# Performance work log

Measured on AMD Instinct MI355X. Metric: run time of the kernel, lower is better.

Reference implementation:

```python
import jax, jax.numpy as jnp
import numpy as np

EPS = 1e-7  # keras.backend.epsilon()


def setup_inputs() -> dict:
    key = jax.random.key(0)
    k1, k2, k3 = jax.random.split(key, 3)
    B, N, D_in, C, D_out = 32, 2048, 8, 32, 16
    x = jax.random.normal(k1, (B, N, D_in), dtype=jnp.float32)
    W = jax.random.normal(k2, (1, N, C, D_out, D_in), dtype=jnp.float32) * 0.05
    R = jax.random.normal(k3, (1, N, C), dtype=jnp.float32)
    return {"x": x, "W": W, "R": R}


def reference(x, W, R):
    # x: [B, N, D_in]; W: [1, N, C, D_out, D_in]; R: [1, N, C]
    R_nor = jax.nn.softmax(R[0], axis=0)          # softmax over N (axis=1 of [1,N,C])
    # per-capsule transform: u[b,n,c,j] = sum_k W[n,c,j,k] * x[b,n,k]
    u = jnp.einsum('ncjk,bnk->bncj', W[0], x)
    # routing-weighted aggregation over input capsules n
    s = jnp.einsum('bncj,nc->bcj', u, R_nor)      # [B, C, D_out]
    # squash along capsule dim (original axis=-2 before squeeze == D_out)
    ss = jnp.sum(jnp.square(s), axis=-1, keepdims=True) + EPS
    scale = jnp.sqrt(ss) / (1.0 + ss)
    return scale * s                               # [B, C, D_out]
```

## Files before the change

kernel.cpp:

```cpp
#include <hip/hip_runtime.h>
#include <math.h>


#define NN 2048
#define CC 32

__device__ __forceinline__ void g2l16(const float* g, float* l) {
  __builtin_amdgcn_global_load_lds((const __attribute__((address_space(1))) void*)g,
                                   (__attribute__((address_space(3))) void*)l, 16, 0, 0);
}

__global__ __launch_bounds__(512) __attribute__((amdgpu_waves_per_eu(4, 4)))
void caps_main(const float* __restrict__ x, const float* __restrict__ W,
               const float* __restrict__ R, float* __restrict__ P) {
  const int bid = blockIdx.x;
  const int cq = bid & 7;
  const int chunk = bid >> 3;
  const int n0 = chunk * 32;
  const int tid = threadIdx.x;
  const int ws = tid >> 6;
  const int lane = tid & 63;
  const int j = lane & 15;
  const int bo = lane >> 4;

  extern __shared__ float smem[];
  float* ldsW = smem;
  float* ldsX = smem + 8192;
  float* red8 = smem + 4096;

#pragma unroll
  for (int it = 0; it < 2; ++it) {
    int idx = it * 512 + tid;
    int nl = idx >> 7, S = idx & 127;
    int g = S ^ (((S >> 2) ^ (S >> 4)) & 1) ^ (((S >> 3) & 1) << 1) ^ (((S >> 4) & 1) << 2);
    g2l16(W + (size_t)(n0 + nl) * 4096 + cq * 512 + g * 4,
          ldsW + (size_t)(it * 512 + ws * 64) * 4);
  }

  float4 xg[4];
  int xoff[4];
#pragma unroll
  for (int it = 0; it < 4; ++it) {
    int idx = it * 512 + tid;
    int nl = idx >> 6, r = idx & 63;
    int b = r & 31, kq = r >> 5;
    xg[it] = *(const float4*)(x + (size_t)b * (NN * 8) + (size_t)(n0 + nl) * 8 + kq * 4);
    xoff[it] = nl * 256 + kq * 128 + b;
  }
#pragma unroll
  for (int it = 0; it < 4; ++it) {
    float* d = ldsX + xoff[it];
    d[0] = xg[it].x; d[32] = xg[it].y; d[64] = xg[it].z; d[96] = xg[it].w;
  }

  float se[4] = {0.f, 0.f, 0.f, 0.f};
#pragma unroll
  for (int i = 0; i < 4; ++i) {
    int n = i * 512 + tid;
    float4 a = *(const float4*)(R + (size_t)n * CC + cq * 4);
    se[0] += expf(a.x); se[1] += expf(a.y); se[2] += expf(a.z); se[3] += expf(a.w);
  }
#pragma unroll
  for (int ci = 0; ci < 4; ++ci) {
    float v = se[ci];
#pragma unroll
    for (int d = 32; d >= 1; d >>= 1) v += __shfl_xor(v, d, 64);
    se[ci] = v;
  }
  if (lane == 0) {
#pragma unroll
    for (int ci = 0; ci < 4; ++ci) red8[ws * 4 + ci] = se[ci];
  }
  __syncthreads();

  float inv4[4];
  {
    float t[4] = {0.f, 0.f, 0.f, 0.f};
#pragma unroll
    for (int w = 0; w < 8; ++w)
#pragma unroll
      for (int ci = 0; ci < 4; ++ci) t[ci] += red8[w * 4 + ci];
#pragma unroll
    for (int ci = 0; ci < 4; ++ci) inv4[ci] = 1.0f / t[ci];
  }
  __syncthreads();

  float acc[4][8];
#pragma unroll
  for (int a = 0; a < 4; ++a)
#pragma unroll
    for (int b = 0; b < 8; ++b) acc[a][b] = 0.f;

  const int jsw = j >> 1;

#pragma unroll 1
  for (int s = 0; s < 4; ++s) {
    if (s < 3) {
      const int sb = n0 + (s + 1) * 8;
      float* wdst = ldsW + (size_t)((s + 1) & 1) * 4096;
#pragma unroll
      for (int it = 0; it < 2; ++it) {
        int idx = it * 512 + tid;
        int nl = idx >> 7, S = idx & 127;
        int g = S ^ (((S >> 2) ^ (S >> 4)) & 1) ^ (((S >> 3) & 1) << 1) ^ (((S >> 4) & 1) << 2);
        g2l16(W + (size_t)(sb + nl) * 4096 + cq * 512 + g * 4,
              wdst + (size_t)(it * 512 + ws * 64) * 4);
      }
    }
    const int n = n0 + s * 8 + ws;
    const float* Xn = ldsX + (size_t)(s * 8 + ws) * 256;
    const float* Wn = ldsW + (size_t)(s & 1) * 4096 + (size_t)ws * 512;

    const float* rr = R + (size_t)n * CC + cq * 4;
    float rv[4];
#pragma unroll
    for (int ci = 0; ci < 4; ++ci) rv[ci] = expf(rr[ci]) * inv4[ci];

#pragma unroll
    for (int kh = 0; kh < 2; ++kh) {
      float4 xlo[4], xhi[4];
#pragma unroll
      for (int kk = 0; kk < 4; ++kk) {
        const float* xp = Xn + (kh * 4 + kk) * 32 + bo * 8;
        xlo[kk] = *(const float4*)xp;
        xhi[kk] = *(const float4*)(xp + 4);
      }
#pragma unroll
      for (int ci = 0; ci < 4; ++ci) {
        int slot = (ci * 32 + j * 2 + kh) ^ jsw;
        float4 wf = *(const float4*)(Wn + slot * 4);
        float rvv = rv[ci];
        float w0 = wf.x * rvv, w1 = wf.y * rvv, w2 = wf.z * rvv, w3 = wf.w * rvv;
        float a0, a1;
#pragma unroll
        for (int bi = 0; bi < 4; ++bi) {
          a0 = acc[ci][bi];
          a0 = fmaf(w0, (&xlo[0].x)[bi], a0);
          a0 = fmaf(w1, (&xlo[1].x)[bi], a0);
          a0 = fmaf(w2, (&xlo[2].x)[bi], a0);
          a0 = fmaf(w3, (&xlo[3].x)[bi], a0);
          acc[ci][bi] = a0;
          a1 = acc[ci][bi + 4];
          a1 = fmaf(w0, (&xhi[0].x)[bi], a1);
          a1 = fmaf(w1, (&xhi[1].x)[bi], a1);
          a1 = fmaf(w2, (&xhi[2].x)[bi], a1);
          a1 = fmaf(w3, (&xhi[3].x)[bi], a1);
          acc[ci][bi + 4] = a1;
        }
      }
    }
    __syncthreads();
  }

  float* red = smem;
#pragma unroll
  for (int half = 4; half >= 1; half >>= 1) {
    if (ws >= half && ws < 2 * half) {
      float* dst = red + (size_t)(ws - half) * 2048;
#pragma unroll
      for (int ci = 0; ci < 4; ++ci)
#pragma unroll
        for (int bi = 0; bi < 8; ++bi)
          dst[(ci * 8 + bi) * 64 + lane] = acc[ci][bi];
    }
    __syncthreads();
    if (ws < half) {
      const float* srcp = red + (size_t)ws * 2048;
#pragma unroll
      for (int ci = 0; ci < 4; ++ci)
#pragma unroll
        for (int bi = 0; bi < 8; ++bi)
          acc[ci][bi] += srcp[(ci * 8 + bi) * 64 + lane];
    }
    __syncthreads();
  }

  if (ws == 0) {
    float* dst = P + (size_t)bid * 2048;
#pragma unroll
    for (int ci = 0; ci < 4; ++ci)
#pragma unroll
      for (int bi = 0; bi < 8; ++bi)
        dst[(ci * 8 + bi) * 64 + lane] = acc[ci][bi];
  }
}

__global__ void caps_reduce(const float* __restrict__ P, float* __restrict__ out) {
  const int g = blockIdx.x * 256 + threadIdx.x;
  const int j = g & 15;
  const int c = (g >> 4) & 31;
  const int b = g >> 9;
  const int bo = b >> 3, bi = b & 7;
  const int cgi = c >> 2, ci = c & 3;
  const int idx = (ci * 8 + bi) * 64 + (bo * 16 + j);

  float s = 0.f;
#pragma unroll 16
  for (int ch = 0; ch < 64; ++ch) {
    s += P[(size_t)(ch * 8 + cgi) * 2048 + idx];
  }
  float sq = s * s;
  sq += __shfl_xor(sq, 8, 16);
  sq += __shfl_xor(sq, 4, 16);
  sq += __shfl_xor(sq, 2, 16);
  sq += __shfl_xor(sq, 1, 16);
  float ss = sq + 1e-7f;
  float scale = sqrtf(ss) / (1.0f + ss);
  out[g] = scale * s;
}

extern "C" void kernel_launch(void* const* d_in, const int* in_sizes, int n_in,
                              void* d_out, int out_size, void* d_ws, size_t ws_size,
                              hipStream_t stream) {
  const float* x = (const float*)d_in[0];
  const float* W = (const float*)d_in[1];
  const float* R = (const float*)d_in[2];
  float* out = (float*)d_out;
  float* P = (float*)d_ws;

  hipFuncSetAttribute((const void*)caps_main,
                      hipFuncAttributeMaxDynamicSharedMemorySize, 65536);

  caps_main<<<512, 512, 65536, stream>>>(x, W, R, P);
  caps_reduce<<<64, 256, 0, stream>>>(P, out);
}
```

Baseline: 28.42 us.

## Replace tree LDS reduction with single-pass float4 reduction and remap block indexing

The end-of-kernel cross-wave reduction used to be a three-level tree with six barriers. It becomes a single pass: all eight waves write their partials to LDS, then every thread sums eight float4 values and writes them to the workspace cooperatively. This cuts barrier count and serial reduction steps, at the cost of more LDS traffic. Block-to-work mapping also changes so consecutive blocks cover consecutive n-chunks for the same capsule group, which changes W/R locality and the workspace layout that the reduce kernel reads.

```diff
diff --git a/kernel.cpp b/kernel.cpp
--- a/kernel.cpp
+++ b/kernel.cpp
@@ -14,8 +14,8 @@
 void caps_main(const float* __restrict__ x, const float* __restrict__ W,
                const float* __restrict__ R, float* __restrict__ P) {
   const int bid = blockIdx.x;
-  const int cq = bid & 7;
-  const int chunk = bid >> 3;
+  const int cq = bid >> 6;
+  const int chunk = bid & 63;
   const int n0 = chunk * 32;
   const int tid = threadIdx.x;
   const int ws = tid >> 6;
@@ -152,36 +152,23 @@
     __syncthreads();
   }
 
-  float* red = smem;
-#pragma unroll
-  for (int half = 4; half >= 1; half >>= 1) {
-    if (ws >= half && ws < 2 * half) {
-      float* dst = red + (size_t)(ws - half) * 2048;
-#pragma unroll
-      for (int ci = 0; ci < 4; ++ci)
-#pragma unroll
-        for (int bi = 0; bi < 8; ++bi)
-          dst[(ci * 8 + bi) * 64 + lane] = acc[ci][bi];
+  float* ldsAll = smem;
+#pragma unroll
+  for (int ci = 0; ci < 4; ++ci)
+#pragma unroll
+    for (int bi = 0; bi < 8; ++bi)
+      ldsAll[(size_t)ws * 2048 + (ci * 8 + bi) * 64 + lane] = acc[ci][bi];
+  __syncthreads();
+
+  {
+    const int t4 = tid * 4;
+    float4 ssum = make_float4(0.f, 0.f, 0.f, 0.f);
+#pragma unroll
+    for (int w = 0; w < 8; ++w) {
+      float4 v = *(const float4*)(ldsAll + (size_t)w * 2048 + t4);
+      ssum.x += v.x; ssum.y += v.y; ssum.z += v.z; ssum.w += v.w;
     }
-    __syncthreads();
-    if (ws < half) {
-      const float* srcp = red + (size_t)ws * 2048;
-#pragma unroll
-      for (int ci = 0; ci < 4; ++ci)
-#pragma unroll
-        for (int bi = 0; bi < 8; ++bi)
-          acc[ci][bi] += srcp[(ci * 8 + bi) * 64 + lane];
-    }
-    __syncthreads();
-  }
-
-  if (ws == 0) {
-    float* dst = P + (size_t)bid * 2048;
-#pragma unroll
-    for (int ci = 0; ci < 4; ++ci)
-#pragma unroll
-      for (int bi = 0; bi < 8; ++bi)
-        dst[(ci * 8 + bi) * 64 + lane] = acc[ci][bi];
+    *(float4*)(P + (size_t)bid * 2048 + t4) = ssum;
   }
 }
 
@@ -191,13 +178,14 @@
   const int c = (g >> 4) & 31;
   const int b = g >> 9;
   const int bo = b >> 3, bi = b & 7;
-  const int cgi = c >> 2, ci = c & 3;
+  const int cq = c >> 2, ci = c & 3;
   const int idx = (ci * 8 + bi) * 64 + (bo * 16 + j);
+  const float* Pq = P + (size_t)cq * 64 * 2048 + idx;
 
   float s = 0.f;
 #pragma unroll 16
   for (int ch = 0; ch < 64; ++ch) {
-    s += P[(size_t)(ch * 8 + cgi) * 2048 + idx];
+    s += Pq[(size_t)ch * 2048];
   }
   float sq = s * s;
   sq += __shfl_xor(sq, 8, 16);
```

After: 40.74 us. 1.43x slower.
